# Kernel optimization log

Hardware: AMD Instinct MI355X
Metric: run time of the kernel (lower is better)

Reference implementation:

```python
import jax, jax.numpy as jnp
import numpy as np

B, C, H, W = 8, 128, 64, 64


def conv1x1(x, w, b):
    # x: [B,C,H,W], w: [Cout,Cin], b: [Cout] -> [B,Cout,H,W]
    return jnp.einsum('bchw,oc->bohw', x, w) + b[None, :, None, None]


def setup_inputs() -> dict:
    key = jax.random.key(0)
    ks = jax.random.split(key, 8)
    scale = 1.0 / np.sqrt(C)  # keep QK logits in a sane range
    return {
        'cur': jax.random.normal(ks[0], (B, C, H, W), jnp.float32),
        'ref': jax.random.normal(ks[1], (B, C, H, W), jnp.float32),
        'theta_w': jax.random.normal(ks[2], (C, C), jnp.float32) * scale,
        'theta_b': jnp.zeros((C,), jnp.float32),
        'phi_w': jax.random.normal(ks[3], (C, C), jnp.float32) * scale,
        'phi_b': jnp.zeros((C,), jnp.float32),
        'W_w': jax.random.normal(ks[4], (C, C), jnp.float32) * scale,
        'W_b': jnp.zeros((C,), jnp.float32),
    }


def reference(cur, ref, theta_w, theta_b, phi_w, phi_b, W_w, W_b):
    b, c, h, w = cur.shape
    n = h * w
    # x = theta(ref): [B, N, C]  (queries come from the reference frame)
    x = conv1x1(ref, theta_w, theta_b).reshape(b, c, n).transpose(0, 2, 1)
    # y = phi(cur): [B, C, N]
    y = conv1x1(cur, phi_w, phi_b).reshape(b, c, n)
    # attn: [B, N_ref, N_cur], softmax over the NON-standard axis 1 (ref positions)
    attn = jax.nn.softmax(jnp.einsum('bnc,bcm->bnm', x, y), axis=1)
    # z = attn @ x: [B, N, C] -> [B, C, H, W]
    z = jnp.einsum('bnm,bmc->bnc', attn, x).transpose(0, 2, 1).reshape(b, c, h, w)
    return conv1x1(z, W_w, W_b)
```

## Files before the change

### kernel.cpp

```cpp
#include <hip/hip_runtime.h>
#include <hip/hip_bf16.h>

#define BB 8
#define CC 128
#define NN 4096
#define LOG2E 1.44269504088896340736f

typedef __attribute__((ext_vector_type(8))) short bf16x8;
typedef __attribute__((ext_vector_type(16))) float f32x16;

static __device__ __forceinline__ unsigned short f2bfu(float f) {
  unsigned int x = __float_as_uint(f);
  x += 0x7fffu + ((x >> 16) & 1u);
  return (unsigned short)(x >> 16);
}
static __device__ __forceinline__ unsigned int packbf(float a, float b) {
  return (unsigned int)f2bfu(a) | ((unsigned int)f2bfu(b) << 16);
}
static __device__ __forceinline__ float bfu2f(unsigned short u) {
  return __uint_as_float((unsigned int)u << 16);
}
static __device__ __forceinline__ f32x16 zero16() {
  f32x16 z;
#pragma unroll
  for (int i = 0; i < 16; ++i) z[i] = 0.f;
  return z;
}
union Frag { int i[4]; unsigned int u[4]; bf16x8 v; };

static __device__ __forceinline__ unsigned int cvtpk(float a, float b) {
  unsigned int r;
  asm("v_cvt_pk_bf16_f32 %0, %1, %2" : "=v"(r) : "v"(a), "v"(b));
  return r;
}
static __device__ __forceinline__ void pl32swap(unsigned int& d, unsigned int& s) {
  asm volatile("v_permlane32_swap_b32 %0, %1" : "+v"(d), "+v"(s));
}

#define GLD16(gp, lp)                                                     \
  __builtin_amdgcn_global_load_lds(                                       \
      (const __attribute__((address_space(1))) unsigned int*)(gp),        \
      (__attribute__((address_space(3))) unsigned int*)(lp), 16, 0, 0)

#define ROWPAT(rg, q2) (((rg) & 3) + 8 * ((rg) >> 2) + 4 * (q2))

static __device__ __forceinline__ void make_pa(const f32x16& s, Frag& lo, Frag& hi) {
  float p[16];
#pragma unroll
  for (int rg = 0; rg < 16; ++rg) p[rg] = exp2f(s[rg]);
  unsigned int a0 = cvtpk(p[0], p[1]),   b0 = cvtpk(p[4], p[5]);
  pl32swap(a0, b0);
  unsigned int a1 = cvtpk(p[2], p[3]),   b1 = cvtpk(p[6], p[7]);
  pl32swap(a1, b1);
  lo.u[0] = a0; lo.u[1] = a1; lo.u[2] = b0; lo.u[3] = b1;
  unsigned int c0 = cvtpk(p[8], p[9]),   d0 = cvtpk(p[12], p[13]);
  pl32swap(c0, d0);
  unsigned int c1 = cvtpk(p[10], p[11]), d1 = cvtpk(p[14], p[15]);
  pl32swap(c1, d1);
  hi.u[0] = c0; hi.u[1] = c1; hi.u[2] = d0; hi.u[3] = d1;
}

__global__ __launch_bounds__(256) void nl_conv2m(
    const float* __restrict__ ref, const float* __restrict__ theta_w,
    const float* __restrict__ theta_b,
    const float* __restrict__ cur, const float* __restrict__ phi_w,
    const float* __restrict__ phi_b,
    unsigned short* __restrict__ Xnc, unsigned short* __restrict__ Xcn,
    unsigned short* __restrict__ Ync)
{
  __shared__ float sm[64 * 129];
  const int z  = blockIdx.z;
  const float* in   = z ? cur : ref;
  const float* w    = z ? phi_w : theta_w;
  const float* bias = z ? phi_b : theta_b;
  unsigned short* out_nc = z ? Ync : Xnc;
  unsigned short* out_cn = z ? nullptr : Xcn;
  const float nc_scale = z ? 1.0f : LOG2E;

  const int b  = blockIdx.y;
  const int n0 = blockIdx.x * 64;
  const int t  = threadIdx.x;
  const int wave = t >> 6, lane = t & 63, q2 = lane >> 5, cm = lane & 31;

#pragma unroll
  for (int k = 0; k < 16; ++k) {
    int flat = t + 256 * k;
    int c = flat >> 5, jp = flat & 31;
    float2 v = *(const float2*)&in[(size_t)b * CC * NN + (size_t)c * NN + n0 + jp * 2];
    sm[c * 64 + jp * 2]     = v.x;
    sm[c * 64 + jp * 2 + 1] = v.y;
  }

  bf16x8 wf[8];
  const int o0 = wave * 32 + cm;
#pragma unroll
  for (int k = 0; k < 8; ++k) {
    const float* wp = &w[o0 * CC + k * 16 + q2 * 8];
    float4 w0 = *(const float4*)wp, w1 = *(const float4*)(wp + 4);
    Frag f;
    f.u[0] = packbf(w0.x, w0.y); f.u[1] = packbf(w0.z, w0.w);
    f.u[2] = packbf(w1.x, w1.y); f.u[3] = packbf(w1.z, w1.w);
    wf[k] = f.v;
  }
  __syncthreads();

  f32x16 acc[2];
  acc[0] = zero16(); acc[1] = zero16();
#pragma unroll
  for (int k = 0; k < 8; ++k) {
#pragma unroll
    for (int jt = 0; jt < 2; ++jt) {
      int base = (k * 16 + q2 * 8) * 64 + jt * 32 + cm;
      Frag xb;
      xb.u[0] = cvtpk(sm[base],       sm[base + 64]);
      xb.u[1] = cvtpk(sm[base + 128], sm[base + 192]);
      xb.u[2] = cvtpk(sm[base + 256], sm[base + 320]);
      xb.u[3] = cvtpk(sm[base + 384], sm[base + 448]);
      acc[jt] = __builtin_amdgcn_mfma_f32_32x32x16_bf16(wf[k], xb.v, acc[jt], 0, 0, 0);
    }
  }
  __syncthreads();

#pragma unroll
  for (int jt = 0; jt < 2; ++jt)
#pragma unroll
    for (int rg = 0; rg < 16; ++rg) {
      int o = wave * 32 + ROWPAT(rg, q2);
      sm[(jt * 32 + cm) * 129 + o] = acc[jt][rg] + bias[o];
    }
  __syncthreads();

#pragma unroll
  for (int k = 0; k < 16; ++k) {
    int flat = t + 256 * k;
    int cp = flat & 63, jj = flat >> 6;
    float f0 = sm[jj * 129 + cp * 2] * nc_scale;
    float f1 = sm[jj * 129 + cp * 2 + 1] * nc_scale;
    *(unsigned int*)(out_nc + ((size_t)b * NN + n0 + jj) * CC + cp * 2) = packbf(f0, f1);
  }
  if (out_cn) {
#pragma unroll
    for (int k = 0; k < 16; ++k) {
      int flat = t + 256 * k;
      int jp = flat & 31, c = flat >> 5;
      float f0 = sm[(jp * 2) * 129 + c], f1 = sm[(jp * 2 + 1) * 129 + c];
      *(unsigned int*)(out_cn + ((size_t)b * CC + c) * NN + n0 + jp * 2) = packbf(f0, f1);
    }
  }
}

__global__ __launch_bounds__(256, 3) void nl_stats4(
    const unsigned short* __restrict__ Xnc, const unsigned short* __restrict__ Ync,
    float* __restrict__ Lpart)
{
  __shared__ unsigned short Xt[2][64 * 128];
  __shared__ float sL[2][2][2][32];
  const int b = blockIdx.z, nq = blockIdx.y, mstrip = blockIdx.x;
  const int t = threadIdx.x;
  const int wave = t >> 6, lane = t & 63, q2 = lane >> 5, cm = lane & 31;
  const int mq = wave & 1, nh = wave >> 1;
  const int m0w = mstrip * 128 + mq * 64;

  bf16x8 bf[2][8];
#pragma unroll
  for (int ct = 0; ct < 2; ++ct)
#pragma unroll
    for (int k = 0; k < 8; ++k)
      bf[ct][k] = *(const bf16x8*)(Ync + ((size_t)b * NN + m0w + ct * 32 + cm) * CC + k * 16 + q2 * 8);

  {
    const int n0 = nq * 1024;
#pragma unroll
    for (int i = 0; i < 4; ++i) {
      int slot = i * 256 + t;
      int row = slot >> 4, g = (slot & 15) ^ (row & 7);
      GLD16(Xnc + ((size_t)b * NN + n0 + row) * CC + g * 8, &Xt[0][0] + i * 2048 + wave * 512);
    }
  }

  float runL[2] = {0.f, 0.f};
#pragma unroll 2
  for (int nt = 0; nt < 16; ++nt) {
    __syncthreads();
    if (nt < 15) {
      const int n0 = nq * 1024 + (nt + 1) * 64;
      unsigned short* dst = &Xt[(nt + 1) & 1][0];
#pragma unroll
      for (int i = 0; i < 4; ++i) {
        int slot = i * 256 + t;
        int row = slot >> 4, g = (slot & 15) ^ (row & 7);
        GLD16(Xnc + ((size_t)b * NN + n0 + row) * CC + g * 8, dst + i * 2048 + wave * 512);
      }
    }
    const unsigned short* src = &Xt[nt & 1][0];
    f32x16 acc0 = zero16(), acc1 = zero16();
#pragma unroll
    for (int k = 0; k < 8; ++k) {
      bf16x8 av = *(const bf16x8*)&src[(nh * 32 + cm) * 128 + (((k << 1) | q2) ^ (cm & 7)) * 8];
      acc0 = __builtin_amdgcn_mfma_f32_32x32x16_bf16(av, bf[0][k], acc0, 0, 0, 0);
      acc1 = __builtin_amdgcn_mfma_f32_32x32x16_bf16(av, bf[1][k], acc1, 0, 0, 0);
    }
#pragma unroll
    for (int rg = 0; rg < 16; ++rg) {
      runL[0] += exp2f(acc0[rg]);
      runL[1] += exp2f(acc1[rg]);
    }
  }
#pragma unroll
  for (int ct = 0; ct < 2; ++ct) runL[ct] += __shfl_xor(runL[ct], 32);
  if (q2 == 0) {
    sL[nh][mq][0][cm] = runL[0];
    sL[nh][mq][1][cm] = runL[1];
  }
  __syncthreads();
  if (t < 128) {
    int mq2 = t >> 6, ct2 = (t >> 5) & 1, cm2 = t & 31;
    float L = sL[0][mq2][ct2][cm2] + sL[1][mq2][ct2][cm2];
    Lpart[((size_t)nq * BB + b) * NN + mstrip * 128 + mq2 * 64 + ct2 * 32 + cm2] = L;
  }
}

__global__ __launch_bounds__(256) void nl_scalev(
    const float* __restrict__ Lp, unsigned short* __restrict__ Xcn)
{
  __shared__ float iL[128];
  const int b = blockIdx.y, mc = blockIdx.x;
  const int t = threadIdx.x;
  const int m0 = mc * 128;
  if (t < 128) {
    size_t idx = (size_t)b * NN + m0 + t;
    float L = Lp[idx] + Lp[(size_t)BB * NN + idx] + Lp[(size_t)2 * BB * NN + idx] +
              Lp[(size_t)3 * BB * NN + idx];
    iL[t] = 1.0f / L;
  }
  __syncthreads();
#pragma unroll
  for (int r = 0; r < 8; ++r) {
    int idx = r * 256 + t;
    int c = idx >> 4, mg = idx & 15;
    size_t base = ((size_t)b * CC + c) * NN + m0 + mg * 8;
    Frag x; x.v = *(const bf16x8*)(Xcn + base);
    const float* il = &iL[mg * 8];
    Frag o;
    o.u[0] = packbf(bfu2f(x.u[0] & 0xffff) * il[0], bfu2f(x.u[0] >> 16) * il[1]);
    o.u[1] = packbf(bfu2f(x.u[1] & 0xffff) * il[2], bfu2f(x.u[1] >> 16) * il[3]);
    o.u[2] = packbf(bfu2f(x.u[2] & 0xffff) * il[4], bfu2f(x.u[2] >> 16) * il[5]);
    o.u[3] = packbf(bfu2f(x.u[3] & 0xffff) * il[6], bfu2f(x.u[3] >> 16) * il[7]);
    *(bf16x8*)(Xcn + base) = o.v;
  }
}

__global__ __launch_bounds__(256, 2) void nl_pass2e2(
    const unsigned short* __restrict__ Xnc, const unsigned short* __restrict__ Ync,
    const unsigned short* __restrict__ Xsc,
    unsigned short* __restrict__ Zpart)
{
  __shared__ unsigned short Yt[2][64 * 128];
  __shared__ unsigned short Xv[2][128 * 64];
  const int b = blockIdx.z, mhalf = blockIdx.y, nstrip = blockIdx.x;
  const int t = threadIdx.x;
  const int wave = t >> 6, lane = t & 63, q2 = lane >> 5, cm = lane & 31;

  bf16x8 af[8];
#pragma unroll
  for (int k = 0; k < 8; ++k)
    af[k] = *(const bf16x8*)(Xnc +
        ((size_t)b * NN + nstrip * 128 + wave * 32 + cm) * CC + k * 16 + q2 * 8);

  f32x16 z[4];
#pragma unroll
  for (int ct = 0; ct < 4; ++ct) z[ct] = zero16();

  {
    const int m0g = mhalf * 2048;
#pragma unroll
    for (int i = 0; i < 4; ++i) {
      int slot = i * 256 + t;
      int row = slot >> 4, g = (slot & 15) ^ (row & 7);
      GLD16(Ync + ((size_t)b * NN + m0g + row) * CC + g * 8, &Yt[0][0] + i * 2048 + wave * 512);
    }
#pragma unroll
    for (int i = 0; i < 4; ++i) {
      int slot = i * 256 + t;
      int row = slot >> 3, g = (slot & 7) ^ (row & 7);
      GLD16(Xsc + ((size_t)b * CC + row) * NN + m0g + g * 8, &Xv[0][0] + i * 2048 + wave * 512);
    }
  }

#define P2_ITER(BUF, MT)                                                       \
  do {                                                                         \
    __syncthreads();                                                           \
    if ((MT) < 31) {                                                           \
      const int m0g = mhalf * 2048 + ((MT) + 1) * 64;                          \
      unsigned short* Yd = &Yt[(BUF) ^ 1][0];                                  \
      unsigned short* Xd = &Xv[(BUF) ^ 1][0];                                  \
      _Pragma("unroll")                                                        \
      for (int i = 0; i < 4; ++i) {                                            \
        int slot = i * 256 + t;                                                \
        int row = slot >> 4, g = (slot & 15) ^ (row & 7);                      \
        GLD16(Ync + ((size_t)b * NN + m0g + row) * CC + g * 8,                 \
              Yd + i * 2048 + wave * 512);                                     \
      }                                                                        \
      _Pragma("unroll")                                                        \
      for (int i = 0; i < 4; ++i) {                                            \
        int slot = i * 256 + t;                                                \
        int row = slot >> 3, g = (slot & 7) ^ (row & 7);                       \
        GLD16(Xsc + ((size_t)b * CC + row) * NN + m0g + g * 8,                 \
              Xd + i * 2048 + wave * 512);                                     \
      }                                                                        \
    }                                                                          \
    const unsigned short* Ys = &Yt[BUF][0];                                    \
    f32x16 s0 = zero16(), s1 = zero16();                                       \
    __builtin_amdgcn_s_setprio(1);                                             \
    _Pragma("unroll")                                                          \
    for (int k = 0; k < 8; ++k) {                                              \
      const int ch = (((k << 1) | q2) ^ (cm & 7)) * 8;                         \
      bf16x8 av0 = *(const bf16x8*)&Ys[cm * 128 + ch];                         \
      bf16x8 av1 = *(const bf16x8*)&Ys[(32 + cm) * 128 + ch];                  \
      s0 = __builtin_amdgcn_mfma_f32_32x32x16_bf16(av0, af[k], s0, 0, 0, 0);   \
      s1 = __builtin_amdgcn_mfma_f32_32x32x16_bf16(av1, af[k], s1, 0, 0, 0);   \
    }                                                                          \
    __builtin_amdgcn_s_setprio(0);                                             \
    Frag pa[4];                                                                \
    make_pa(s0, pa[0], pa[1]);                                                 \
    make_pa(s1, pa[2], pa[3]);                                                 \
    const unsigned short* Xs = &Xv[BUF][0];                                    \
    __builtin_amdgcn_s_setprio(1);                                             \
    _Pragma("unroll")                                                          \
    for (int ks = 0; ks < 4; ++ks) {                                           \
      const int ch = (((ks << 1) | q2) ^ (cm & 7)) * 8;                        \
      _Pragma("unroll")                                                        \
      for (int ct = 0; ct < 4; ++ct) {                                         \
        bf16x8 xv = *(const bf16x8*)&Xs[(ct * 32 + cm) * 64 + ch];             \
        z[ct] = __builtin_amdgcn_mfma_f32_32x32x16_bf16(pa[ks].v, xv, z[ct], 0, 0, 0); \
      }                                                                        \
    }                                                                          \
    __builtin_amdgcn_s_setprio(0);                                             \
  } while (0)

  for (int mt2 = 0; mt2 < 16; ++mt2) {
    P2_ITER(0, mt2 * 2);
    P2_ITER(1, mt2 * 2 + 1);
  }
#undef P2_ITER

  unsigned short* Zp = Zpart + ((size_t)mhalf * BB + b) * NN * CC;
#pragma unroll
  for (int ct = 0; ct < 4; ++ct)
#pragma unroll
    for (int rg = 0; rg < 16; ++rg) {
      int n = nstrip * 128 + wave * 32 + ROWPAT(rg, q2);
      Zp[(size_t)n * CC + ct * 32 + cm] = f2bfu(z[ct][rg]);
    }
}

__global__ __launch_bounds__(256) void nl_convw2(
    const unsigned short* __restrict__ Zpart, const float* __restrict__ w,
    const float* __restrict__ bias, float* __restrict__ out)
{
  __shared__ unsigned short Zt[128 * 128];
  const int b = blockIdx.y, nstrip = blockIdx.x;
  const int t = threadIdx.x;
  const int wave = t >> 6, lane = t & 63, q2 = lane >> 5, cm = lane & 31;
  const int oh = wave & 1, nh2 = wave >> 1;

  const unsigned short* Z0 = Zpart + ((size_t)b * NN + nstrip * 128) * CC;
  const unsigned short* Z1 = Z0 + (size_t)BB * NN * CC;
#pragma unroll
  for (int i = 0; i < 8; ++i) {
    int slot = i * 256 + t;
    int row = slot >> 4, g = slot & 15;
    size_t off = (size_t)row * CC + g * 8;
    Frag a, c2, o;
    a.v  = *(const bf16x8*)(Z0 + off);
    c2.v = *(const bf16x8*)(Z1 + off);
#pragma unroll
    for (int w2 = 0; w2 < 4; ++w2) {
      float lo = bfu2f((unsigned short)(a.u[w2] & 0xffff)) +
                 bfu2f((unsigned short)(c2.u[w2] & 0xffff));
      float hi = bfu2f((unsigned short)(a.u[w2] >> 16)) +
                 bfu2f((unsigned short)(c2.u[w2] >> 16));
      o.u[w2] = packbf(lo, hi);
    }
    *(bf16x8*)&Zt[row * 128 + ((g ^ (row & 7)) * 8)] = o.v;
  }

  bf16x8 wf[2][8];
#pragma unroll
  for (int s2 = 0; s2 < 2; ++s2)
#pragma unroll
    for (int k = 0; k < 8; ++k) {
      const float* wp = &w[(oh * 64 + s2 * 32 + cm) * CC + k * 16 + q2 * 8];
      float4 w0 = *(const float4*)wp, w1 = *(const float4*)(wp + 4);
      Frag f;
      f.u[0] = packbf(w0.x, w0.y); f.u[1] = packbf(w0.z, w0.w);
      f.u[2] = packbf(w1.x, w1.y); f.u[3] = packbf(w1.z, w1.w);
      wf[s2][k] = f.v;
    }
  __syncthreads();

  f32x16 z[2][2];
  z[0][0] = zero16(); z[0][1] = zero16(); z[1][0] = zero16(); z[1][1] = zero16();
#pragma unroll
  for (int k = 0; k < 8; ++k) {
    bf16x8 bv[2];
#pragma unroll
    for (int j = 0; j < 2; ++j)
      bv[j] = *(const bf16x8*)&Zt[(nh2 * 64 + j * 32 + cm) * 128 + (((k << 1) | q2) ^ (cm & 7)) * 8];
#pragma unroll
    for (int i = 0; i < 2; ++i)
#pragma unroll
      for (int j = 0; j < 2; ++j)
        z[i][j] = __builtin_amdgcn_mfma_f32_32x32x16_bf16(wf[i][k], bv[j], z[i][j], 0, 0, 0);
  }

#pragma unroll
  for (int i = 0; i < 2; ++i)
#pragma unroll
    for (int rg = 0; rg < 16; ++rg) {
      int o = oh * 64 + i * 32 + ROWPAT(rg, q2);
      float bv2 = bias[o];
#pragma unroll
      for (int j = 0; j < 2; ++j) {
        int n = nstrip * 128 + nh2 * 64 + j * 32 + cm;
        out[(size_t)b * CC * NN + (size_t)o * NN + n] = z[i][j][rg] + bv2;
      }
    }
}

extern "C" void kernel_launch(void* const* d_in, const int* in_sizes, int n_in,
                              void* d_out, int out_size, void* d_ws, size_t ws_size,
                              hipStream_t stream) {
  const float* cur     = (const float*)d_in[0];
  const float* ref     = (const float*)d_in[1];
  const float* theta_w = (const float*)d_in[2];
  const float* theta_b = (const float*)d_in[3];
  const float* phi_w   = (const float*)d_in[4];
  const float* phi_b   = (const float*)d_in[5];
  const float* Ww      = (const float*)d_in[6];
  const float* Wb      = (const float*)d_in[7];
  float* out = (float*)d_out;

  unsigned short* Xnc = (unsigned short*)d_ws;
  unsigned short* Ync = Xnc + (size_t)BB * NN * CC;
  unsigned short* Xcn = Ync + (size_t)BB * NN * CC;
  float* Lpart = (float*)(Xcn + (size_t)BB * NN * CC);
  unsigned short* Zpart = (unsigned short*)(Lpart + (size_t)4 * BB * NN);

  dim3 blk(256);
  nl_conv2m  <<<dim3(64, BB, 2), blk, 0, stream>>>(ref, theta_w, theta_b,
                                                   cur, phi_w, phi_b, Xnc, Xcn, Ync);
  nl_stats4  <<<dim3(32, 4, BB), blk, 0, stream>>>(Xnc, Ync, Lpart);
  nl_scalev  <<<dim3(32, BB), blk, 0, stream>>>(Lpart, Xcn);
  nl_pass2e2 <<<dim3(32, 2, BB), blk, 0, stream>>>(Xnc, Ync, Xcn, Zpart);
  nl_convw2  <<<dim3(32, BB), blk, 0, stream>>>(Zpart, Ww, Wb, out);
}
```

Baseline: 262.0 us.

## Use raw exp2 intrinsic, raise occupancy bounds, halve tiles in scale and W-conv kernels

Replaces exp2f with the hardware exp2 builtin in the softmax statistics and probability paths, dropping the library wrapper's range handling. Raises launch_bounds occupancy hints on the conv and stats kernels. Halves the per-block tile in the scale and final 1x1 conv kernels and doubles their grids, so more blocks run on the 256 CUs at the cost of reloading W-conv weights per smaller block. The raw exp2 may differ slightly on denormal or extreme inputs.

New measurement: 231.4 us. -11.7%, faster.

```diff
diff --git a/kernel.cpp b/kernel.cpp
--- a/kernel.cpp
+++ b/kernel.cpp
@@ -20,6 +20,9 @@
 static __device__ __forceinline__ float bfu2f(unsigned short u) {
   return __uint_as_float((unsigned int)u << 16);
 }
+static __device__ __forceinline__ float fexp2(float x) {
+  return __builtin_amdgcn_exp2f(x);
+}
 static __device__ __forceinline__ f32x16 zero16() {
   f32x16 z;
 #pragma unroll
@@ -47,7 +50,7 @@
 static __device__ __forceinline__ void make_pa(const f32x16& s, Frag& lo, Frag& hi) {
   float p[16];
 #pragma unroll
-  for (int rg = 0; rg < 16; ++rg) p[rg] = exp2f(s[rg]);
+  for (int rg = 0; rg < 16; ++rg) p[rg] = fexp2(s[rg]);
   unsigned int a0 = cvtpk(p[0], p[1]),   b0 = cvtpk(p[4], p[5]);
   pl32swap(a0, b0);
   unsigned int a1 = cvtpk(p[2], p[3]),   b1 = cvtpk(p[6], p[7]);
@@ -60,7 +63,7 @@
   hi.u[0] = c0; hi.u[1] = c1; hi.u[2] = d0; hi.u[3] = d1;
 }
 
-__global__ __launch_bounds__(256) void nl_conv2m(
+__global__ __launch_bounds__(256, 4) void nl_conv2m(
     const float* __restrict__ ref, const float* __restrict__ theta_w,
     const float* __restrict__ theta_b,
     const float* __restrict__ cur, const float* __restrict__ phi_w,
@@ -149,7 +152,7 @@
   }
 }
 
-__global__ __launch_bounds__(256, 3) void nl_stats4(
+__global__ __launch_bounds__(256, 4) void nl_stats4(
     const unsigned short* __restrict__ Xnc, const unsigned short* __restrict__ Ync,
     float* __restrict__ Lpart)
 {
@@ -202,8 +205,8 @@
     }
 #pragma unroll
     for (int rg = 0; rg < 16; ++rg) {
-      runL[0] += exp2f(acc0[rg]);
-      runL[1] += exp2f(acc1[rg]);
+      runL[0] += fexp2(acc0[rg]);
+      runL[1] += fexp2(acc1[rg]);
     }
   }
 #pragma unroll
@@ -223,11 +226,11 @@
 __global__ __launch_bounds__(256) void nl_scalev(
     const float* __restrict__ Lp, unsigned short* __restrict__ Xcn)
 {
-  __shared__ float iL[128];
+  __shared__ float iL[64];
   const int b = blockIdx.y, mc = blockIdx.x;
   const int t = threadIdx.x;
-  const int m0 = mc * 128;
-  if (t < 128) {
+  const int m0 = mc * 64;
+  if (t < 64) {
     size_t idx = (size_t)b * NN + m0 + t;
     float L = Lp[idx] + Lp[(size_t)BB * NN + idx] + Lp[(size_t)2 * BB * NN + idx] +
               Lp[(size_t)3 * BB * NN + idx];
@@ -235,9 +238,9 @@
   }
   __syncthreads();
 #pragma unroll
-  for (int r = 0; r < 8; ++r) {
+  for (int r = 0; r < 4; ++r) {
     int idx = r * 256 + t;
-    int c = idx >> 4, mg = idx & 15;
+    int c = idx >> 3, mg = idx & 7;
     size_t base = ((size_t)b * CC + c) * NN + m0 + mg * 8;
     Frag x; x.v = *(const bf16x8*)(Xcn + base);
     const float* il = &iL[mg * 8];
@@ -358,16 +361,16 @@
     const unsigned short* __restrict__ Zpart, const float* __restrict__ w,
     const float* __restrict__ bias, float* __restrict__ out)
 {
-  __shared__ unsigned short Zt[128 * 128];
+  __shared__ unsigned short Zt[64 * 128];
   const int b = blockIdx.y, nstrip = blockIdx.x;
   const int t = threadIdx.x;
   const int wave = t >> 6, lane = t & 63, q2 = lane >> 5, cm = lane & 31;
   const int oh = wave & 1, nh2 = wave >> 1;
 
-  const unsigned short* Z0 = Zpart + ((size_t)b * NN + nstrip * 128) * CC;
+  const unsigned short* Z0 = Zpart + ((size_t)b * NN + nstrip * 64) * CC;
   const unsigned short* Z1 = Z0 + (size_t)BB * NN * CC;
 #pragma unroll
-  for (int i = 0; i < 8; ++i) {
+  for (int i = 0; i < 4; ++i) {
     int slot = i * 256 + t;
     int row = slot >> 4, g = slot & 15;
     size_t off = (size_t)row * CC + g * 8;
@@ -399,19 +402,14 @@
     }
   __syncthreads();
 
-  f32x16 z[2][2];
-  z[0][0] = zero16(); z[0][1] = zero16(); z[1][0] = zero16(); z[1][1] = zero16();
+  f32x16 z[2];
+  z[0] = zero16(); z[1] = zero16();
 #pragma unroll
   for (int k = 0; k < 8; ++k) {
-    bf16x8 bv[2];
-#pragma unroll
-    for (int j = 0; j < 2; ++j)
-      bv[j] = *(const bf16x8*)&Zt[(nh2 * 64 + j * 32 + cm) * 128 + (((k << 1) | q2) ^ (cm & 7)) * 8];
+    bf16x8 bv = *(const bf16x8*)&Zt[(nh2 * 32 + cm) * 128 + (((k << 1) | q2) ^ (cm & 7)) * 8];
 #pragma unroll
     for (int i = 0; i < 2; ++i)
-#pragma unroll
-      for (int j = 0; j < 2; ++j)
-        z[i][j] = __builtin_amdgcn_mfma_f32_32x32x16_bf16(wf[i][k], bv[j], z[i][j], 0, 0, 0);
+      z[i] = __builtin_amdgcn_mfma_f32_32x32x16_bf16(wf[i][k], bv, z[i], 0, 0, 0);
   }
 
 #pragma unroll
@@ -419,12 +417,8 @@
 #pragma unroll
     for (int rg = 0; rg < 16; ++rg) {
       int o = oh * 64 + i * 32 + ROWPAT(rg, q2);
-      float bv2 = bias[o];
-#pragma unroll
-      for (int j = 0; j < 2; ++j) {
-        int n = nstrip * 128 + nh2 * 64 + j * 32 + cm;
-        out[(size_t)b * CC * NN + (size_t)o * NN + n] = z[i][j][rg] + bv2;
-      }
+      int n = nstrip * 64 + nh2 * 32 + cm;
+      out[(size_t)b * CC * NN + (size_t)o * NN + n] = z[i][rg] + bias[o];
     }
 }
 
@@ -451,7 +445,7 @@
   nl_conv2m  <<<dim3(64, BB, 2), blk, 0, stream>>>(ref, theta_w, theta_b,
                                                    cur, phi_w, phi_b, Xnc, Xcn, Ync);
   nl_stats4  <<<dim3(32, 4, BB), blk, 0, stream>>>(Xnc, Ync, Lpart);
-  nl_scalev  <<<dim3(32, BB), blk, 0, stream>>>(Lpart, Xcn);
+  nl_scalev  <<<dim3(64, BB), blk, 0, stream>>>(Lpart, Xcn);
   nl_pass2e2 <<<dim3(32, 2, BB), blk, 0, stream>>>(Xnc, Ync, Xcn, Zpart);
-  nl_convw2  <<<dim3(32, BB), blk, 0, stream>>>(Zpart, Ww, Wb, out);
-}
+  nl_convw2  <<<dim3(64, BB), blk, 0, stream>>>(Zpart, Ww, Wb, out);
+}
```
